# Kernel optimization log

Hardware: AMD Instinct MI355X
Metric: run time of the kernel (lower is better)

Reference implementation:

```python
import jax, jax.numpy as jnp
import numpy as np

D = 1024      # d_model
H = 16        # n_heads
HD = D // H   # head_dim = 64
B = 2
T = 2048


def setup_inputs() -> dict:
    key = jax.random.key(0)
    k0, k1, k2 = jax.random.split(key, 3)
    s = 1.0 / np.sqrt(D)
    return {
        "x": jax.random.normal(k0, (B, T, D), dtype=jnp.float32),
        "qkv_w": jax.random.normal(k1, (D, 3 * D), dtype=jnp.float32) * s,
        "qkv_b": jnp.zeros((3 * D,), dtype=jnp.float32),
        "out_w": jax.random.normal(k2, (D, D), dtype=jnp.float32) * s,
        "out_b": jnp.zeros((D,), dtype=jnp.float32),
    }


def _apply_rotary(x, rope):
    # Faithful to the torch apply_rotary: even/odd interleaved split of both
    # x and the [sin(freqs)|cos(freqs)] rope table.
    x1, x2 = x[..., ::2], x[..., 1::2]
    sin, cos = rope[..., ::2], rope[..., 1::2]
    return jnp.concatenate([x1 * cos - x2 * sin, x1 * sin + x2 * cos], axis=-1)


def reference(x, qkv_w, qkv_b, out_w, out_b):
    Bx, Tx, Dm = x.shape
    # QKV projection -> [3, B, H, T, HD]
    qkv = (x @ qkv_w + qkv_b).reshape(Bx, Tx, 3, H, HD).transpose(2, 0, 3, 1, 4)
    q, k, v = qkv[0], qkv[1], qkv[2]

    # Rotary table: rope = concat(sin(freqs), cos(freqs)) along last dim -> [T, HD]
    inv_freq = 1.0 / (10000.0 ** (jnp.arange(0, HD, 2, dtype=jnp.float32) / HD))
    t = jnp.arange(Tx, dtype=jnp.float32)
    freqs = t[:, None] * inv_freq[None, :]          # [T, HD/2]
    rope = jnp.concatenate([jnp.sin(freqs), jnp.cos(freqs)], axis=-1)  # [T, HD]

    q = _apply_rotary(q, rope)
    k = _apply_rotary(k, rope)

    scale = HD ** -0.5
    scores = jnp.einsum('bhqd,bhkd->bhqk', q, k) * scale  # [B,H,T,T]
    causal_mask = jnp.triu(jnp.ones((Tx, Tx), dtype=bool), 1)
    scores = jnp.where(causal_mask, -jnp.inf, scores)
    attn = jax.nn.softmax(scores, axis=-1)
    # dropout is identity in eval mode
    out = jnp.einsum('bhqk,bhkd->bhqd', attn, v)           # [B,H,T,HD]
    out = out.transpose(0, 2, 1, 3).reshape(Bx, Tx, Dm)    # [B,T,D]
    return out @ out_w + out_b
```

## Files before the change

kernel.cpp:

```cpp
#include <hip/hip_runtime.h>

typedef unsigned short u16;
typedef __attribute__((ext_vector_type(8))) __bf16 bf16x8;
typedef __attribute__((ext_vector_type(4))) float f32x4;

#define NB 2
#define NT 2048
#define ND 1024
#define NH 16
#define HD 64

__device__ __forceinline__ float b2f(u16 u) {
  union { float f; unsigned int i; } v; v.i = ((unsigned int)u) << 16; return v.f;
}
__device__ __forceinline__ u16 f2b(float f) {
  union { float f; unsigned int i; } v; v.f = f;
  unsigned int r = (v.i + 0x7FFFu + ((v.i >> 16) & 1u)) >> 16;
  return (u16)r;
}

__device__ __forceinline__ void gload_lds16(const u16* g, u16* lds) {
  __builtin_amdgcn_global_load_lds(
      (const __attribute__((address_space(1))) unsigned int*)(g),
      (__attribute__((address_space(3))) unsigned int*)(lds),
      16, 0, 0);
}

__device__ __forceinline__ f32x4 mfma16(bf16x8 a, bf16x8 b, f32x4 c) {
  return __builtin_amdgcn_mfma_f32_16x16x32_bf16(a, b, c, 0, 0, 0);
}

template <int N>
__device__ __forceinline__ float ror16(float x) {
  return __int_as_float(__builtin_amdgcn_update_dpp(
      __float_as_int(x), __float_as_int(x), 0x120 | N, 0xF, 0xF, true));
}
__device__ __forceinline__ float rsum16(float x) {
  x += ror16<8>(x);
  x += ror16<4>(x);
  x += ror16<2>(x);
  x += ror16<1>(x);
  return x;
}

__device__ __forceinline__ float fast_sin(float a) {
  float r = a * 0.15915494309189535f;
  r -= floorf(r);
  return __builtin_amdgcn_sinf(r);
}
__device__ __forceinline__ float fast_cos(float a) {
  float r = a * 0.15915494309189535f;
  r -= floorf(r);
  return __builtin_amdgcn_cosf(r);
}

__global__ __launch_bounds__(256) void cast_f32_bf16(const float* __restrict__ in,
                                                     u16* __restrict__ out, int n) {
  int i = (blockIdx.x * 256 + threadIdx.x) * 8;
  if (i + 8 <= n) {
#pragma unroll
    for (int j = 0; j < 8; ++j) out[i + j] = f2b(in[i + j]);
  }
}

__global__ __launch_bounds__(256) void transpose_cast(const float* __restrict__ in,
                                                      u16* __restrict__ out,
                                                      int K, int N) {
  __shared__ u16 tile[32][33];
  int n0 = blockIdx.x * 32, k0 = blockIdx.y * 32;
  int tx = threadIdx.x, ty = threadIdx.y;
  for (int i = ty; i < 32; i += 8)
    tile[i][tx] = f2b(in[(size_t)(k0 + i) * N + n0 + tx]);
  __syncthreads();
  for (int i = ty; i < 32; i += 8)
    out[(size_t)(n0 + i) * K + k0 + tx] = tile[tx][i];
}

template <int BM, bool F32OUT>
__global__ __launch_bounds__(256) void gemm_bt(const u16* __restrict__ A,
                                               const u16* __restrict__ Bt,
                                               const float* __restrict__ bias,
                                               void* __restrict__ Cv,
                                               int M, int N, int K) {
  constexpr int MI = BM / 32;
  __shared__ alignas(16) u16 As[BM * 32];
  __shared__ alignas(16) u16 Bs[128 * 32];
  const int tid = threadIdx.x;
  const int lane = tid & 63;
  const int wave = tid >> 6;
  const int l15 = lane & 15, quad = lane >> 4;
  const int wm = (wave >> 1) * (BM / 2), wn = (wave & 1) * 64;
  const int row0 = blockIdx.y * BM, col0 = blockIdx.x * 128;

  f32x4 acc[MI][4] = {};

  for (int k0 = 0; k0 < K; k0 += 32) {
    __syncthreads();
#pragma unroll
    for (int p = 0; p < BM / 64; ++p) {
      int idx8 = p * 256 + tid;
      int r = idx8 >> 2, c = (idx8 & 3) * 8;
      gload_lds16(&A[(size_t)(row0 + r) * K + k0 + c], &As[idx8 * 8]);
    }
#pragma unroll
    for (int p = 0; p < 2; ++p) {
      int idx8 = p * 256 + tid;
      int r = idx8 >> 2, c = (idx8 & 3) * 8;
      gload_lds16(&Bt[(size_t)(col0 + r) * K + k0 + c], &Bs[idx8 * 8]);
    }
    __syncthreads();
    bf16x8 af[MI], bfr[4];
#pragma unroll
    for (int mi = 0; mi < MI; ++mi)
      af[mi] = *(const bf16x8*)&As[(wm + mi * 16 + l15) * 32 + quad * 8];
#pragma unroll
    for (int ni = 0; ni < 4; ++ni)
      bfr[ni] = *(const bf16x8*)&Bs[(wn + ni * 16 + l15) * 32 + quad * 8];
#pragma unroll
    for (int mi = 0; mi < MI; ++mi)
#pragma unroll
      for (int ni = 0; ni < 4; ++ni)
        acc[mi][ni] = mfma16(af[mi], bfr[ni], acc[mi][ni]);
  }

#pragma unroll
  for (int ni = 0; ni < 4; ++ni) {
    int c = col0 + wn + ni * 16 + l15;
    float bv = bias[c];
#pragma unroll
    for (int mi = 0; mi < MI; ++mi) {
      int r0 = row0 + wm + mi * 16 + quad * 4;
      f32x4 v = acc[mi][ni];
#pragma unroll
      for (int r = 0; r < 4; ++r) {
        if (F32OUT)
          ((float*)Cv)[(size_t)(r0 + r) * N + c] = v[r] + bv;
        else
          ((u16*)Cv)[(size_t)(r0 + r) * N + c] = f2b(v[r] + bv);
      }
    }
  }
}

__device__ __forceinline__ void stage_half(const u16* __restrict__ g, int ldk,
                                           u16* l, int tid) {
#pragma unroll
  for (int p = 0; p < 2; ++p) {
    int idx = p * 512 + tid;
    int r = idx >> 3;
    int c = (idx & 7) ^ (r & 7);
    gload_lds16(&g[(size_t)r * ldk + c * 8], &l[idx * 8]);
  }
}

#define AH(b, h) (&lds[((b) * 2 + (h)) * 8192])
#define BH(b, h) (&lds[32768 + ((b) * 2 + (h)) * 8192])

#define LOAD_AF(base)                                                       \
  _Pragma("unroll") for (int mm = 0; mm < 4; ++mm) {                        \
    af[mm][0] = *(const bf16x8*)&(base)[arow + mm * 2048 + swz0];           \
    af[mm][1] = *(const bf16x8*)&(base)[arow + mm * 2048 + swz1];           \
  }
#define LOAD_BF(base)                                                       \
  _Pragma("unroll") for (int nn = 0; nn < 2; ++nn) {                        \
    bfr[nn][0] = *(const bf16x8*)&(base)[brow + nn * 4096 + swz0];          \
    bfr[nn][1] = *(const bf16x8*)&(base)[brow + nn * 4096 + swz1];          \
  }
#define MFMA_Q(MA, NQ)                                                      \
  _Pragma("unroll") for (int mm = 0; mm < 4; ++mm)                          \
  _Pragma("unroll") for (int nn = 0; nn < 2; ++nn) {                        \
    acc[(MA) * 4 + mm][(NQ) * 2 + nn] =                                     \
        mfma16(af[mm][0], bfr[nn][0], acc[(MA) * 4 + mm][(NQ) * 2 + nn]);   \
    acc[(MA) * 4 + mm][(NQ) * 2 + nn] =                                     \
        mfma16(af[mm][1], bfr[nn][1], acc[(MA) * 4 + mm][(NQ) * 2 + nn]);   \
  }
#define PH_SYNC                                                             \
  __builtin_amdgcn_s_barrier();                                             \
  asm volatile("s_waitcnt lgkmcnt(0)");                                     \
  __builtin_amdgcn_sched_barrier(0);                                        \
  __builtin_amdgcn_s_setprio(1);
#define PH_END                                                              \
  __builtin_amdgcn_s_setprio(0);                                            \
  __builtin_amdgcn_s_barrier();                                             \
  asm volatile("" ::: "memory");

__global__ __launch_bounds__(512, 2) void gemm256_bt(const u16* __restrict__ A,
                                                     const u16* __restrict__ Bt,
                                                     const float* __restrict__ bias,
                                                     u16* __restrict__ C,
                                                     int M, int N, int K) {
  __shared__ alignas(16) u16 lds[65536];
  const int tid = threadIdx.x;
  const int lane = tid & 63;
  const int wave = tid >> 6;
  const int l15 = lane & 15, quad = lane >> 4;
  const int wm = wave >> 2, wn = wave & 3;
  const int row0 = blockIdx.y * 256, col0 = blockIdx.x * 256;
  const int NTIL = K >> 6;

  const u16* Ag0 = A + (size_t)row0 * K;
  const u16* Ag1 = Ag0 + (size_t)128 * K;
  const u16* Bg0 = Bt + (size_t)col0 * K;
  const u16* Bg1 = Bg0 + (size_t)128 * K;

  const int swz0 = (quad ^ (l15 & 7)) * 8;
  const int swz1 = ((4 + quad) ^ (l15 & 7)) * 8;
  const int arow = (wm * 16 + l15) * 64;
  const int brow = (wn * 16 + l15) * 64;

  f32x4 acc[8][4] = {};

  stage_half(Bg0, K, BH(0, 0), tid);
  stage_half(Ag1, K, AH(0, 1), tid);
  stage_half(Ag0, K, AH(0, 0), tid);
  stage_half(Bg1, K, BH(0, 1), tid);
  {
    int tp = (NTIL > 1) ? 1 : 0;
    stage_half(Bg0 + tp * 64, K, BH(1, 0), tid);
    stage_half(Ag1 + tp * 64, K, AH(1, 1), tid);
  }
  asm volatile("s_waitcnt vmcnt(4)");
  __builtin_amdgcn_s_barrier();
  asm volatile("" ::: "memory");

  bf16x8 af[4][2], bfr[2][2];
#pragma unroll 2
  for (int t = 0; t < NTIL; ++t) {
    const int cur = t & 1, nxt = cur ^ 1;
    const int t1 = (t + 1 < NTIL) ? t + 1 : NTIL - 1;
    const int t2 = (t + 2 < NTIL) ? t + 2 : NTIL - 1;
    u16* Ac0 = AH(cur, 0);
    u16* Ac1 = AH(cur, 1);
    u16* Bc0 = BH(cur, 0);
    u16* Bc1 = BH(cur, 1);

    LOAD_AF(Ac0);
    LOAD_BF(Bc0);
    stage_half(Ag0 + t1 * 64, K, AH(nxt, 0), tid);
    PH_SYNC; MFMA_Q(0, 0); PH_END;

    LOAD_AF(Ac1);
    stage_half(Bg1 + t1 * 64, K, BH(nxt, 1), tid);
    PH_SYNC; MFMA_Q(1, 0); PH_END;

    LOAD_BF(Bc1);
    stage_half(Bg0 + t2 * 64, K, Bc0, tid);
    PH_SYNC; MFMA_Q(1, 1); PH_END;

    LOAD_AF(Ac0);
    stage_half(Ag1 + t2 * 64, K, Ac1, tid);
    __builtin_amdgcn_s_barrier();
    asm volatile("s_waitcnt lgkmcnt(0)");
    __builtin_amdgcn_sched_barrier(0);
    __builtin_amdgcn_s_setprio(1);
    MFMA_Q(0, 1);
    __builtin_amdgcn_s_setprio(0);
    asm volatile("s_waitcnt vmcnt(4)");
    __builtin_amdgcn_s_barrier();
    asm volatile("" ::: "memory");
  }
  asm volatile("s_waitcnt vmcnt(0)");

#pragma unroll
  for (int ni = 0; ni < 4; ++ni) {
    const int col = col0 + (ni >> 1) * 128 + (ni & 1) * 64 + wn * 16 + l15;
    const float bv = bias[col];
#pragma unroll
    for (int mi = 0; mi < 8; ++mi) {
      const int r0 = row0 + (mi >> 2) * 128 + (mi & 3) * 32 + wm * 16 + quad * 4;
      f32x4 v = acc[mi][ni];
#pragma unroll
      for (int rr = 0; rr < 4; ++rr)
        C[(size_t)(r0 + rr) * N + col] = f2b(v[rr] + bv);
    }
  }
}

__global__ __launch_bounds__(256) void prep_frag(const u16* __restrict__ qkv,
                                                 u16* __restrict__ qsw,
                                                 u16* __restrict__ ksw,
                                                 u16* __restrict__ vsw) {
  __shared__ u16 tq[32 * 72];
  __shared__ u16 tk[32 * 72];
  __shared__ u16 tv[32 * 72];
  const int bh = blockIdx.y;
  const int b = bh >> 4, h = bh & 15;
  const int t0 = blockIdx.x * 32;
  const int tid = threadIdx.x;

  {
    int row = tid >> 3, col = (tid & 7) * 8;
    const u16* src = &qkv[(size_t)(b * NT + t0 + row) * 3072 + h * HD + col];
    *(bf16x8*)&tq[row * 72 + col] = *(const bf16x8*)src;
    *(bf16x8*)&tk[row * 72 + col] = *(const bf16x8*)(src + ND);
    *(bf16x8*)&tv[row * 72 + col] = *(const bf16x8*)(src + 2 * ND);
  }
  __syncthreads();

  {
    const int isK = tid >> 7;
    const int chunk = (tid >> 4) & 7;
    const int tl = tid & 15;
    const int ks = chunk >> 2, quad = chunk & 3;
    const u16* tile = isK ? tk : tq;
    u16* dst = isK ? ksw : qsw;
    const float scale = isK ? 1.0f : 0.125f;
    const float LOG1E4 = 9.210340371976184f;

#pragma unroll
    for (int rbloc = 0; rbloc < 2; ++rbloc) {
      const int row = rbloc * 16 + tl;
      const float tf = (float)(t0 + row);
      union { u16 s[8]; bf16x8 v; } o;
#pragma unroll
      for (int e = 0; e < 8; ++e) {
        int c = ks * 32 + quad * 8 + e;
        int j = c & 31;
        int c1 = 2 * j, c2 = 2 * j + 1;
        float inv1 = __expf(-((float)(c1 & 31)) * (1.0f / 32.0f) * LOG1E4);
        float inv2 = __expf(-((float)(c2 & 31)) * (1.0f / 32.0f) * LOG1E4);
        float a1 = tf * inv1, a2 = tf * inv2;
        float sA = (c1 < 32) ? fast_sin(a1) : fast_cos(a1);
        float cA = (c2 < 32) ? fast_sin(a2) : fast_cos(a2);
        float x1 = b2f(tile[row * 72 + c1]), x2 = b2f(tile[row * 72 + c2]);
        float ov = (c < 32) ? (x1 * cA - x2 * sA) : (x1 * sA + x2 * cA);
        o.s[e] = f2b(ov * scale);
      }
      size_t addr =
          ((((size_t)bh * 128 + (t0 >> 4) + rbloc) * 2 + ks) * 64 + quad * 16 + tl) * 8;
      *(bf16x8*)&dst[addr] = o.v;
    }
  }

  {
    const int ni = tid >> 6, lane = tid & 63;
    const int quad = lane >> 4, l15 = lane & 15;
    union { u16 s[8]; bf16x8 v; } o;
#pragma unroll
    for (int e = 0; e < 8; ++e)
      o.s[e] = tv[(quad * 8 + e) * 72 + ni * 16 + l15];
    *(bf16x8*)&vsw[(((size_t)bh * 64 + (t0 >> 5)) * 4 + ni) * 512 + lane * 8] = o.v;
  }
}

__global__ __launch_bounds__(128, 2) void flash_kernel(const u16* __restrict__ qsw,
                                                       const u16* __restrict__ ksw,
                                                       const u16* __restrict__ vsw,
                                                       u16* __restrict__ attn) {
  __shared__ alignas(16) u16 Ps[2 * 5120];
  __shared__ float Ll[32];

  const int tid = threadIdx.x;
  const int w = tid >> 6;
  const int lane = tid & 63;
  const int l15 = lane & 15, quad = lane >> 4;
  const int linear = (int)blockIdx.x;
  const int bh = linear & 31;
  const int qt = 63 - (linear >> 5);
  const int r0 = qt * 32;
  u16* Psw = &Ps[w * 5120];

  bf16x8 aq[2][2];
#pragma unroll
  for (int mi = 0; mi < 2; ++mi)
#pragma unroll
    for (int ks = 0; ks < 2; ++ks)
      aq[mi][ks] = *(const bf16x8*)&qsw[
          ((((size_t)bh * 128 + qt * 2 + mi) * 2 + ks) * 64 + lane) * 8];

  f32x4 oacc[2][4] = {};
  float lst[8] = {0.f, 0.f, 0.f, 0.f, 0.f, 0.f, 0.f, 0.f};

  const int ktmax = qt >> 2;
  for (int kt = w; kt <= ktmax; kt += 2) {
    bf16x8 kf[2][8];
#pragma unroll
    for (int ks = 0; ks < 2; ++ks)
#pragma unroll
      for (int ni = 0; ni < 8; ++ni)
        kf[ks][ni] = *(const bf16x8*)&ksw[
            ((((size_t)bh * 128 + kt * 8 + ni) * 2 + ks) * 64 + lane) * 8];

    f32x4 sacc[2][8] = {};
#pragma unroll
    for (int ks = 0; ks < 2; ++ks)
#pragma unroll
      for (int ni = 0; ni < 8; ++ni) {
        sacc[0][ni] = mfma16(aq[0][ks], kf[ks][ni], sacc[0][ni]);
        sacc[1][ni] = mfma16(aq[1][ks], kf[ks][ni], sacc[1][ni]);
      }

    bf16x8 vf[4][4];
#pragma unroll
    for (int ks = 0; ks < 4; ++ks)
#pragma unroll
      for (int ni = 0; ni < 4; ++ni)
        vf[ks][ni] = *(const bf16x8*)&vsw[
            (((size_t)bh * 64 + kt * 4 + ks) * 4 + ni) * 512 + lane * 8];

    const bool diag = (kt == ktmax);
    const int k0 = kt * 128;
#pragma unroll
    for (int mi = 0; mi < 2; ++mi)
#pragma unroll
      for (int r = 0; r < 4; ++r) {
        const int prow = mi * 16 + quad * 4 + r;
        float sv[8];
#pragma unroll
        for (int ni = 0; ni < 8; ++ni) sv[ni] = sacc[mi][ni][r];
        if (diag) {
#pragma unroll
          for (int ni = 0; ni < 8; ++ni)
            if (k0 + ni * 16 + l15 > r0 + prow) sv[ni] = -__builtin_inff();
        }
        float rs = 0.f;
#pragma unroll
        for (int ni = 0; ni < 8; ++ni) {
          float p = __expf(sv[ni]);
          sv[ni] = p;
          rs += p;
        }
        lst[mi * 4 + r] += rsum16(rs);
#pragma unroll
        for (int ni = 0; ni < 8; ++ni)
          Psw[(ni >> 1) * 1280 + prow * 40 + (ni & 1) * 16 + l15] = f2b(sv[ni]);
      }

    asm volatile("" ::: "memory");

#pragma unroll
    for (int ks = 0; ks < 4; ++ks) {
      bf16x8 ap0 = *(const bf16x8*)&Psw[ks * 1280 + l15 * 40 + quad * 8];
      bf16x8 ap1 = *(const bf16x8*)&Psw[ks * 1280 + (16 + l15) * 40 + quad * 8];
#pragma unroll
      for (int ni = 0; ni < 4; ++ni) {
        oacc[0][ni] = mfma16(ap0, vf[ks][ni], oacc[0][ni]);
        oacc[1][ni] = mfma16(ap1, vf[ks][ni], oacc[1][ni]);
      }
    }
  }

  float* Of = (float*)&Ps[5120];
  if (w == 1) {
#pragma unroll
    for (int mi = 0; mi < 2; ++mi)
#pragma unroll
      for (int r = 0; r < 4; ++r) {
        const int row = mi * 16 + quad * 4 + r;
        if (l15 == 0) Ll[row] = lst[mi * 4 + r];
#pragma unroll
        for (int ni = 0; ni < 4; ++ni)
          Of[row * 64 + ni * 16 + l15] = oacc[mi][ni][r];
      }
  }
  __syncthreads();
  if (w == 0) {
    const int b = bh >> 4, h = bh & 15;
#pragma unroll
    for (int mi = 0; mi < 2; ++mi)
#pragma unroll
      for (int r = 0; r < 4; ++r) {
        const int row = mi * 16 + quad * 4 + r;
        const float rl = 1.0f / (lst[mi * 4 + r] + Ll[row]);
        const int trow = r0 + row;
#pragma unroll
        for (int ni = 0; ni < 4; ++ni) {
          float o = oacc[mi][ni][r] + Of[row * 64 + ni * 16 + l15];
          attn[((size_t)b * NT + trow) * ND + h * HD + ni * 16 + l15] = f2b(o * rl);
        }
      }
  }
}

extern "C" void kernel_launch(void* const* d_in, const int* in_sizes, int n_in,
                              void* d_out, int out_size, void* d_ws, size_t ws_size,
                              hipStream_t stream) {
  const float* x = (const float*)d_in[0];
  const float* qkv_w = (const float*)d_in[1];
  const float* qkv_b = (const float*)d_in[2];
  const float* out_w = (const float*)d_in[3];
  const float* out_b = (const float*)d_in[4];
  float* out = (float*)d_out;

  u16* ws = (u16*)d_ws;
  u16* xb    = ws;
  u16* wqkvT = xb + (size_t)4096 * 1024;
  u16* woutT = wqkvT + 3072 * 1024;
  u16* qkv   = woutT + 1024 * 1024;
  u16* qsw   = qkv + (size_t)4096 * 3072;
  u16* ksw   = qsw + (size_t)32 * 2048 * 64;
  u16* vsw   = ksw + (size_t)32 * 2048 * 64;
  u16* attn  = vsw + (size_t)32 * 2048 * 64;

  cast_f32_bf16<<<(NB * NT * ND) / (256 * 8), 256, 0, stream>>>(
      x, xb, NB * NT * ND);

  transpose_cast<<<dim3(3 * ND / 32, ND / 32), dim3(32, 8), 0, stream>>>(
      qkv_w, wqkvT, ND, 3 * ND);
  transpose_cast<<<dim3(ND / 32, ND / 32), dim3(32, 8), 0, stream>>>(
      out_w, woutT, ND, ND);

  gemm256_bt<<<dim3(3 * ND / 256, NB * NT / 256), 512, 0, stream>>>(
      xb, wqkvT, qkv_b, qkv, NB * NT, 3 * ND, ND);

  prep_frag<<<dim3(NT / 32, NB * NH), 256, 0, stream>>>(qkv, qsw, ksw, vsw);

  flash_kernel<<<dim3(2048), 128, 0, stream>>>(qsw, ksw, vsw, attn);

  gemm_bt<64, true><<<dim3(ND / 128, NB * NT / 64), 256, 0, stream>>>(
      attn, woutT, out_b, out, NB * NT, ND, ND);
}
```

Baseline: 190.2 us.

## Double-buffer output projection GEMM with 128x128 tiles and XCD-aware block swizzle

Replaces the simple single-buffered output-projection GEMM with a 128x128-tile kernel. It uses K=64 double-buffered LDS staging with XOR swizzle and sets occupancy to 2 blocks per CU. It also adds an XCD-aware workgroup remapping to both GEMMs so neighbouring tiles share L2. The staging address arithmetic in the QKV GEMM is precomputed. The output GEMM now launches fewer blocks (256), which may underfill the CUs, and it uses more LDS per block.

```diff
diff --git a/kernel.cpp b/kernel.cpp
--- a/kernel.cpp
+++ b/kernel.cpp
@@ -28,6 +28,12 @@
 
 __device__ __forceinline__ f32x4 mfma16(bf16x8 a, bf16x8 b, f32x4 c) {
   return __builtin_amdgcn_mfma_f32_16x16x32_bf16(a, b, c, 0, 0, 0);
+}
+
+__device__ __forceinline__ int xcd_swizzle(int lin, int nwg) {
+  int q = nwg >> 3, r = nwg & 7;
+  int xcd = lin & 7, loc = lin >> 3;
+  return (xcd < r ? xcd * (q + 1) : r * (q + 1) + (xcd - r) * q) + loc;
 }
 
 template <int N>
@@ -76,81 +82,95 @@
     out[(size_t)(n0 + i) * K + k0 + tx] = tile[tx][i];
 }
 
-template <int BM, bool F32OUT>
-__global__ __launch_bounds__(256) void gemm_bt(const u16* __restrict__ A,
-                                               const u16* __restrict__ Bt,
-                                               const float* __restrict__ bias,
-                                               void* __restrict__ Cv,
-                                               int M, int N, int K) {
-  constexpr int MI = BM / 32;
-  __shared__ alignas(16) u16 As[BM * 32];
-  __shared__ alignas(16) u16 Bs[128 * 32];
+__global__ __launch_bounds__(256, 2) void gemm128_2ph(const u16* __restrict__ A,
+                                                      const u16* __restrict__ Bt,
+                                                      const float* __restrict__ bias,
+                                                      float* __restrict__ C,
+                                                      int M, int N, int K) {
+  __shared__ alignas(16) u16 lds[2][2][8192];
   const int tid = threadIdx.x;
   const int lane = tid & 63;
   const int wave = tid >> 6;
   const int l15 = lane & 15, quad = lane >> 4;
-  const int wm = (wave >> 1) * (BM / 2), wn = (wave & 1) * 64;
-  const int row0 = blockIdx.y * BM, col0 = blockIdx.x * 128;
-
-  f32x4 acc[MI][4] = {};
-
-  for (int k0 = 0; k0 < K; k0 += 32) {
-    __syncthreads();
-#pragma unroll
-    for (int p = 0; p < BM / 64; ++p) {
-      int idx8 = p * 256 + tid;
-      int r = idx8 >> 2, c = (idx8 & 3) * 8;
-      gload_lds16(&A[(size_t)(row0 + r) * K + k0 + c], &As[idx8 * 8]);
+  const int wm = (wave >> 1) * 64, wn = (wave & 1) * 64;
+
+  const int gx = gridDim.x;
+  const int nwg = gx * gridDim.y;
+  const int swz = xcd_swizzle(blockIdx.y * gx + blockIdx.x, nwg);
+  const int row0 = (swz / gx) * 128, col0 = (swz % gx) * 128;
+
+  const int sr = tid >> 3;
+  const size_t soff = (size_t)sr * K + (size_t)((tid & 7) ^ (sr & 7)) * 8;
+  const u16* Ab = A + (size_t)row0 * K;
+  const u16* Bb = Bt + (size_t)col0 * K;
+
+  const int swz0 = (quad ^ (l15 & 7)) * 8;
+  const int swz1 = ((4 + quad) ^ (l15 & 7)) * 8;
+  const int arow = (wm + l15) * 64;
+  const int brow = (wn + l15) * 64;
+
+  f32x4 acc[4][4] = {};
+  const int NTIL = K >> 6;
+
+#define STAGE8(dst, bptr, koff)                                              \
+  _Pragma("unroll") for (int p = 0; p < 4; ++p)                              \
+      gload_lds16((bptr) + (koff) + soff + (size_t)p * 32 * K,               \
+                  &(dst)[(p * 256 + tid) * 8]);
+
+  STAGE8(lds[0][0], Ab, 0);
+  STAGE8(lds[0][1], Bb, 0);
+  asm volatile("s_waitcnt vmcnt(0)");
+  __builtin_amdgcn_s_barrier();
+  asm volatile("" ::: "memory");
+
+  for (int t = 0; t < NTIL; ++t) {
+    const int cur = t & 1;
+    if (t + 1 < NTIL) {
+      STAGE8(lds[cur ^ 1][0], Ab, (size_t)(t + 1) * 64);
+      STAGE8(lds[cur ^ 1][1], Bb, (size_t)(t + 1) * 64);
     }
-#pragma unroll
-    for (int p = 0; p < 2; ++p) {
-      int idx8 = p * 256 + tid;
-      int r = idx8 >> 2, c = (idx8 & 3) * 8;
-      gload_lds16(&Bt[(size_t)(col0 + r) * K + k0 + c], &Bs[idx8 * 8]);
+    bf16x8 af[4][2], bfr[4][2];
+#pragma unroll
+    for (int i = 0; i < 4; ++i) {
+      af[i][0]  = *(const bf16x8*)&lds[cur][0][arow + i * 1024 + swz0];
+      af[i][1]  = *(const bf16x8*)&lds[cur][0][arow + i * 1024 + swz1];
+      bfr[i][0] = *(const bf16x8*)&lds[cur][1][brow + i * 1024 + swz0];
+      bfr[i][1] = *(const bf16x8*)&lds[cur][1][brow + i * 1024 + swz1];
     }
-    __syncthreads();
-    bf16x8 af[MI], bfr[4];
-#pragma unroll
-    for (int mi = 0; mi < MI; ++mi)
-      af[mi] = *(const bf16x8*)&As[(wm + mi * 16 + l15) * 32 + quad * 8];
-#pragma unroll
-    for (int ni = 0; ni < 4; ++ni)
-      bfr[ni] = *(const bf16x8*)&Bs[(wn + ni * 16 + l15) * 32 + quad * 8];
-#pragma unroll
-    for (int mi = 0; mi < MI; ++mi)
-#pragma unroll
-      for (int ni = 0; ni < 4; ++ni)
-        acc[mi][ni] = mfma16(af[mi], bfr[ni], acc[mi][ni]);
-  }
-
-#pragma unroll
-  for (int ni = 0; ni < 4; ++ni) {
-    int c = col0 + wn + ni * 16 + l15;
-    float bv = bias[c];
-#pragma unroll
-    for (int mi = 0; mi < MI; ++mi) {
-      int r0 = row0 + wm + mi * 16 + quad * 4;
-      f32x4 v = acc[mi][ni];
-#pragma unroll
-      for (int r = 0; r < 4; ++r) {
-        if (F32OUT)
-          ((float*)Cv)[(size_t)(r0 + r) * N + c] = v[r] + bv;
-        else
-          ((u16*)Cv)[(size_t)(r0 + r) * N + c] = f2b(v[r] + bv);
-      }
+    asm volatile("s_waitcnt lgkmcnt(0)");
+    __builtin_amdgcn_sched_barrier(0);
+#pragma unroll
+    for (int i = 0; i < 4; ++i)
+#pragma unroll
+      for (int j = 0; j < 4; ++j) {
+        acc[i][j] = mfma16(af[i][0], bfr[j][0], acc[i][j]);
+        acc[i][j] = mfma16(af[i][1], bfr[j][1], acc[i][j]);
+      }
+    asm volatile("s_waitcnt vmcnt(0)");
+    __builtin_amdgcn_s_barrier();
+    asm volatile("" ::: "memory");
+  }
+#undef STAGE8
+
+#pragma unroll
+  for (int j = 0; j < 4; ++j) {
+    const int c = col0 + wn + j * 16 + l15;
+    const float bv = bias[c];
+#pragma unroll
+    for (int i = 0; i < 4; ++i) {
+      const int rr0 = row0 + wm + i * 16 + quad * 4;
+      f32x4 v = acc[i][j];
+#pragma unroll
+      for (int rr = 0; rr < 4; ++rr)
+        C[(size_t)(rr0 + rr) * N + c] = v[rr] + bv;
     }
   }
 }
 
-__device__ __forceinline__ void stage_half(const u16* __restrict__ g, int ldk,
-                                           u16* l, int tid) {
-#pragma unroll
-  for (int p = 0; p < 2; ++p) {
-    int idx = p * 512 + tid;
-    int r = idx >> 3;
-    int c = (idx & 7) ^ (r & 7);
-    gload_lds16(&g[(size_t)r * ldk + c * 8], &l[idx * 8]);
-  }
+__device__ __forceinline__ void stage2(const u16* g0, const u16* g1, u16* l,
+                                       int tid) {
+  gload_lds16(g0, &l[tid * 8]);
+  gload_lds16(g1, &l[(512 + tid) * 8]);
 }
 
 #define AH(b, h) (&lds[((b) * 2 + (h)) * 8192])
@@ -195,13 +215,20 @@
   const int wave = tid >> 6;
   const int l15 = lane & 15, quad = lane >> 4;
   const int wm = wave >> 2, wn = wave & 3;
-  const int row0 = blockIdx.y * 256, col0 = blockIdx.x * 256;
+
+  const int gx = gridDim.x;
+  const int nwg = gx * gridDim.y;
+  const int bswz = xcd_swizzle(blockIdx.y * gx + blockIdx.x, nwg);
+  const int row0 = (bswz / gx) * 256, col0 = (bswz % gx) * 256;
   const int NTIL = K >> 6;
 
-  const u16* Ag0 = A + (size_t)row0 * K;
-  const u16* Ag1 = Ag0 + (size_t)128 * K;
-  const u16* Bg0 = Bt + (size_t)col0 * K;
-  const u16* Bg1 = Bg0 + (size_t)128 * K;
+  const int sr = tid >> 3;
+  const size_t soff = (size_t)sr * K + (size_t)((tid & 7) ^ (sr & 7)) * 8;
+  const size_t hK = (size_t)64 * K;
+  const u16* A0p = A + (size_t)row0 * K + soff;
+  const u16* A1p = A0p + 2 * hK;
+  const u16* B0p = Bt + (size_t)col0 * K + soff;
+  const u16* B1p = B0p + 2 * hK;
 
   const int swz0 = (quad ^ (l15 & 7)) * 8;
   const int swz1 = ((4 + quad) ^ (l15 & 7)) * 8;
@@ -210,14 +237,14 @@
 
   f32x4 acc[8][4] = {};
 
-  stage_half(Bg0, K, BH(0, 0), tid);
-  stage_half(Ag1, K, AH(0, 1), tid);
-  stage_half(Ag0, K, AH(0, 0), tid);
-  stage_half(Bg1, K, BH(0, 1), tid);
+  stage2(B0p, B0p + hK, BH(0, 0), tid);
+  stage2(A1p, A1p + hK, AH(0, 1), tid);
+  stage2(A0p, A0p + hK, AH(0, 0), tid);
+  stage2(B1p, B1p + hK, BH(0, 1), tid);
   {
     int tp = (NTIL > 1) ? 1 : 0;
-    stage_half(Bg0 + tp * 64, K, BH(1, 0), tid);
-    stage_half(Ag1 + tp * 64, K, AH(1, 1), tid);
+    stage2(B0p + tp * 64, B0p + tp * 64 + hK, BH(1, 0), tid);
+    stage2(A1p + tp * 64, A1p + tp * 64 + hK, AH(1, 1), tid);
   }
   asm volatile("s_waitcnt vmcnt(4)");
   __builtin_amdgcn_s_barrier();
@@ -227,8 +254,8 @@
 #pragma unroll 2
   for (int t = 0; t < NTIL; ++t) {
     const int cur = t & 1, nxt = cur ^ 1;
-    const int t1 = (t + 1 < NTIL) ? t + 1 : NTIL - 1;
-    const int t2 = (t + 2 < NTIL) ? t + 2 : NTIL - 1;
+    const int o1 = ((t + 1 < NTIL) ? t + 1 : NTIL - 1) * 64;
+    const int o2 = ((t + 2 < NTIL) ? t + 2 : NTIL - 1) * 64;
     u16* Ac0 = AH(cur, 0);
     u16* Ac1 = AH(cur, 1);
     u16* Bc0 = BH(cur, 0);
@@ -236,19 +263,19 @@
 
     LOAD_AF(Ac0);
     LOAD_BF(Bc0);
-    stage_half(Ag0 + t1 * 64, K, AH(nxt, 0), tid);
+    stage2(A0p + o1, A0p + o1 + hK, AH(nxt, 0), tid);
     PH_SYNC; MFMA_Q(0, 0); PH_END;
 
     LOAD_AF(Ac1);
-    stage_half(Bg1 + t1 * 64, K, BH(nxt, 1), tid);
+    stage2(B1p + o1, B1p + o1 + hK, BH(nxt, 1), tid);
     PH_SYNC; MFMA_Q(1, 0); PH_END;
 
     LOAD_BF(Bc1);
-    stage_half(Bg0 + t2 * 64, K, Bc0, tid);
+    stage2(B0p + o2, B0p + o2 + hK, Bc0, tid);
     PH_SYNC; MFMA_Q(1, 1); PH_END;
 
     LOAD_AF(Ac0);
-    stage_half(Ag1 + t2 * 64, K, Ac1, tid);
+    stage2(A1p + o2, A1p + o2 + hK, Ac1, tid);
     __builtin_amdgcn_s_barrier();
     asm volatile("s_waitcnt lgkmcnt(0)");
     __builtin_amdgcn_sched_barrier(0);
@@ -507,6 +534,6 @@
 
   flash_kernel<<<dim3(2048), 128, 0, stream>>>(qsw, ksw, vsw, attn);
 
-  gemm_bt<64, true><<<dim3(ND / 128, NB * NT / 64), 256, 0, stream>>>(
+  gemm128_2ph<<<dim3(ND / 128, NB * NT / 128), 256, 0, stream>>>(
       attn, woutT, out_b, out, NB * NT, ND, ND);
 }
```

New measurement: 189.7 us. About the same (-0.3%).
